# Performance work log

Measured on AMD Instinct MI355X. Metric: run time of the kernel, lower is better.

Reference implementation:

```python
import jax, jax.numpy as jnp
import numpy as np


def _lin_relu(V, W, b):
    # LinearEmbedding: matmul + bias + ReLU (with_act_func=True default)
    return jax.nn.relu(jnp.matmul(V, W) + b)


def setup_inputs() -> dict:
    key = jax.random.key(0)
    ks = jax.random.split(key, 8)
    B, N, F = 4, 4096, 512
    C = F // 8
    sx = 1.0 / np.sqrt(F)
    return {
        "V": jax.random.normal(ks[0], (B, N, F), dtype=jnp.float32),
        "Wf": jax.random.normal(ks[1], (F, C), dtype=jnp.float32) * sx,
        "bf": jax.random.normal(ks[2], (C,), dtype=jnp.float32) * 5e-5 + 1e-4,
        "Wg": jax.random.normal(ks[3], (F, C), dtype=jnp.float32) * sx,
        "bg": jax.random.normal(ks[4], (C,), dtype=jnp.float32) * 5e-5 + 1e-4,
        "Wh": jax.random.normal(ks[5], (F, F), dtype=jnp.float32) * sx,
        "bh": jax.random.normal(ks[6], (F,), dtype=jnp.float32) * 5e-5 + 1e-4,
        "gamma": jax.random.normal(ks[7], (F,), dtype=jnp.float32),
    }


def reference(V, Wf, bf, Wg, bg, Wh, bh, gamma):
    f_out = _lin_relu(V, Wf, bf)          # [B, N, C]
    g_out = _lin_relu(V, Wg, bg)          # [B, N, C]
    h_out = _lin_relu(V, Wh, bh)          # [B, N, F]
    scores = jnp.einsum('bnc,bmc->bnm', f_out, g_out)  # [B, N, N]
    s = jax.nn.softmax(scores, axis=-1)
    o = jnp.einsum('bnm,bmf->bnf', s, h_out)            # [B, N, F]
    return gamma * o + V
```

## Files before the change

kernel.cpp:

```cpp
#include <hip/hip_runtime.h>
#include <hip/hip_bf16.h>
#include <math.h>

#define M_ROWS 16384
#define F_DIM 512
#define C_DIM 64

typedef short bf16x8 __attribute__((ext_vector_type(8)));
typedef float floatx4 __attribute__((ext_vector_type(4)));
typedef unsigned short ushortx8 __attribute__((ext_vector_type(8)));
typedef unsigned short ushortx4 __attribute__((ext_vector_type(4)));

static __device__ __forceinline__ unsigned short f2bf(float x) {
    __hip_bfloat16 h = __float2bfloat16(x);
    return *reinterpret_cast<unsigned short*>(&h);
}
static __device__ __forceinline__ float bf2f(unsigned short h) {
    unsigned int u = ((unsigned int)h) << 16;
    return __builtin_bit_cast(float, u);
}

static __device__ __forceinline__ void lgkm_barrier() {
    asm volatile("s_waitcnt lgkmcnt(0)\n\ts_barrier" ::: "memory");
}


__global__ __launch_bounds__(64) void prep_w_kernel(
    const float* __restrict__ Wf, const float* __restrict__ Wg,
    const float* __restrict__ Wh,
    unsigned short* __restrict__ wt_hi, unsigned short* __restrict__ wt_lo)
{
    const int c = blockIdx.x;
    const int t = threadIdx.x;
    const float* W; int ld, cl;
    if (c < 64)       { W = Wf; ld = C_DIM; cl = c; }
    else if (c < 128) { W = Wg; ld = C_DIM; cl = c - 64; }
    else              { W = Wh; ld = F_DIM; cl = c - 128; }
    const int ng = c >> 4, l16 = c & 15;
    for (int k = t; k < F_DIM; k += 64) {
        const float x = W[(size_t)k * ld + cl];
        const unsigned short h = f2bf(x);
        const int kh = k >> 5, qd = (k >> 3) & 3, j = k & 7;
        const size_t off = (((size_t)(ng * 16 + kh) * 64) + qd * 16 + l16) * 8 + j;
        wt_hi[off] = h;
        wt_lo[off] = f2bf(x - bf2f(h));
    }
}

#define BM 64
#define LDK 72

__global__ __launch_bounds__(256, 4) void embed_mfma_kernel(
    const float* __restrict__ V,
    const unsigned short* __restrict__ wt_hi, const unsigned short* __restrict__ wt_lo,
    const float* __restrict__ bf, const float* __restrict__ bg,
    const float* __restrict__ bh,
    unsigned short* __restrict__ f_bf, unsigned short* __restrict__ g_bf,
    unsigned short* __restrict__ h_sw)
{
    __shared__ __align__(16) unsigned short a_hi[BM][LDK];
    __shared__ __align__(16) unsigned short a_lo[BM][LDK];

    const int t  = threadIdx.x;
    const int R0 = blockIdx.x * BM;
    const bool fg = (blockIdx.y == 0);
    const int cbase = fg ? 0 : blockIdx.y * 128;

    const int w = t >> 6, lane = t & 63, quad = lane >> 4, l16 = lane & 15;

    floatx4 acc[4][2];
    #pragma unroll
    for (int rt = 0; rt < 4; ++rt)
        #pragma unroll
        for (int c = 0; c < 2; ++c)
            acc[rt][c] = (floatx4){0.f, 0.f, 0.f, 0.f};

    const int arow = t >> 4;
    const int acol = (t & 15) * 4;
    const int ng0  = (cbase >> 4) + w * 2;

    #pragma unroll 1
    for (int k0 = 0; k0 < F_DIM; k0 += 64) {
        lgkm_barrier();
        #pragma unroll
        for (int rr = 0; rr < 4; ++rr) {
            const int row = rr * 16 + arow;
            const float4 x = *(const float4*)(V + (size_t)(R0 + row) * F_DIM + k0 + acol);
            const float xs[4] = {x.x, x.y, x.z, x.w};
            ushortx4 hi, lo;
            #pragma unroll
            for (int jj = 0; jj < 4; ++jj) {
                const unsigned short hb2 = f2bf(xs[jj]);
                hi[jj] = hb2;
                lo[jj] = f2bf(xs[jj] - bf2f(hb2));
            }
            *(ushortx4*)&a_hi[row][acol] = hi;
            if (fg) *(ushortx4*)&a_lo[row][acol] = lo;
        }
        lgkm_barrier();
        #pragma unroll
        for (int kk = 0; kk < 2; ++kk) {
            const int kh = (k0 >> 5) + kk;
            const bf16x8 b0 = *(const bf16x8*)(wt_hi + (((size_t)(ng0 * 16 + kh)) * 64 + lane) * 8);
            const bf16x8 b1 = *(const bf16x8*)(wt_hi + (((size_t)((ng0 + 1) * 16 + kh)) * 64 + lane) * 8);
            bf16x8 ah[4];
            #pragma unroll
            for (int rt = 0; rt < 4; ++rt)
                ah[rt] = *(const bf16x8*)&a_hi[rt * 16 + l16][kk * 32 + quad * 8];
            #pragma unroll
            for (int rt = 0; rt < 4; ++rt) {
                acc[rt][0] = __builtin_amdgcn_mfma_f32_16x16x32_bf16(ah[rt], b0, acc[rt][0], 0, 0, 0);
                acc[rt][1] = __builtin_amdgcn_mfma_f32_16x16x32_bf16(ah[rt], b1, acc[rt][1], 0, 0, 0);
            }
            if (fg) {
                const bf16x8 c0 = *(const bf16x8*)(wt_lo + (((size_t)(ng0 * 16 + kh)) * 64 + lane) * 8);
                const bf16x8 c1 = *(const bf16x8*)(wt_lo + (((size_t)((ng0 + 1) * 16 + kh)) * 64 + lane) * 8);
                bf16x8 al[4];
                #pragma unroll
                for (int rt = 0; rt < 4; ++rt)
                    al[rt] = *(const bf16x8*)&a_lo[rt * 16 + l16][kk * 32 + quad * 8];
                #pragma unroll
                for (int rt = 0; rt < 4; ++rt) {
                    acc[rt][0] = __builtin_amdgcn_mfma_f32_16x16x32_bf16(ah[rt], c0, acc[rt][0], 0, 0, 0);
                    acc[rt][0] = __builtin_amdgcn_mfma_f32_16x16x32_bf16(al[rt], b0, acc[rt][0], 0, 0, 0);
                    acc[rt][1] = __builtin_amdgcn_mfma_f32_16x16x32_bf16(ah[rt], c1, acc[rt][1], 0, 0, 0);
                    acc[rt][1] = __builtin_amdgcn_mfma_f32_16x16x32_bf16(al[rt], b1, acc[rt][1], 0, 0, 0);
                }
            }
        }
    }

    #pragma unroll
    for (int rt = 0; rt < 4; ++rt) {
        #pragma unroll
        for (int c = 0; c < 2; ++c) {
            const int wtc  = cbase + w * 32 + c * 16 + l16;
            const int rowl = rt * 16 + quad * 4;
            const float bias = fg ? (wtc < 64 ? bf[wtc] : bg[wtc - 64]) : bh[wtc - 128];
            const floatx4 v = acc[rt][c];
            if (fg) {
                unsigned short* dst = (wtc < 64) ? (f_bf + wtc) : (g_bf + wtc - 64);
                #pragma unroll
                for (int r = 0; r < 4; ++r) {
                    const float z = v[r] + bias;
                    dst[(size_t)(R0 + rowl + r) * C_DIM] = f2bf(z > 0.f ? z : 0.f);
                }
            } else {
                const int hc   = wtc - 128;
                const int grow = R0 + rowl;
                const int b    = grow >> 12, rl = grow & 4095;
                const int T    = rl >> 6, mloc = rl & 63;
                const int kh2  = mloc >> 5, q2 = (mloc >> 3) & 3, j0 = mloc & 7;
                ushortx4 st;
                #pragma unroll
                for (int r = 0; r < 4; ++r) {
                    const float z = v[r] + bias;
                    st[r] = f2bf(z > 0.f ? z : 0.f);
                }
                const size_t off = ((((size_t)(b * 64 + T) * 64) + (hc >> 4) * 2 + kh2) * 64
                                    + q2 * 16 + (hc & 15)) * 8 + j0;
                *(ushortx4*)(h_sw + off) = st;
            }
        }
    }
}

#define QT 128
#define KT 64
#define PST 72
#define GST 72

__global__ __launch_bounds__(1024, 4) void attn_mfma_kernel(
    const unsigned short* __restrict__ f_bf, const unsigned short* __restrict__ g_bf,
    const unsigned short* __restrict__ h_sw,
    unsigned short* __restrict__ O_ws, float* __restrict__ l_ws)
{
    __shared__ __align__(16) unsigned short p_lds[2][QT][PST];
    __shared__ __align__(16) unsigned short g_lds[2][KT][GST];
    __shared__ __align__(16) float l_half[2][QT];

    const int t = threadIdx.x;
    const int w = t >> 6, lane = t & 63, quad = lane >> 4, l16 = lane & 15;
    const int sr = (w & 7) * 16, sc = (w >> 3) * 32;

    const int bid = blockIdx.x;
    const int b   = (bid & 7) >> 1;
    const int j   = ((bid >> 3) << 1) | (bid & 1);
    const int qb  = j >> 1;
    const int ms  = j & 1;
    const int R0  = qb * QT;
    const int M0  = ms * 2048;

    const unsigned short* fb = f_bf + ((size_t)b * 4096 + R0) * C_DIM;
    const unsigned short* gb = g_bf + ((size_t)b * 4096 + M0) * C_DIM;
    const unsigned short* hbase = h_sw + (size_t)(b * 64 + ms * 32) * 32768;

    bf16x8 f0, f1;
    {
        const unsigned short* fr = fb + (size_t)(sr + l16) * C_DIM + quad * 8;
        f0 = *(const bf16x8*)fr;
        f1 = *(const bf16x8*)(fr + 32);
    }

    floatx4 acc[8][2];
    #pragma unroll
    for (int rt = 0; rt < 8; ++rt)
        #pragma unroll
        for (int c = 0; c < 2; ++c)
            acc[rt][c] = (floatx4){0.f, 0.f, 0.f, 0.f};
    float run_l[4] = {0.f, 0.f, 0.f, 0.f};

    const int grow = t >> 4, gk = (t & 15) * 4;
    ushortx4 greg = *(const ushortx4*)(gb + (size_t)grow * C_DIM + gk);

    for (int it = 0; it < 32; ++it) {
        const int buf = it & 1;
        const unsigned short* ht = hbase + (size_t)it * 32768 + (size_t)(4 * w) * 512;

        const bf16x8 h0 = *(const bf16x8*)(ht + (size_t)lane * 8);
        const bf16x8 h1 = *(const bf16x8*)(ht + 512 + (size_t)lane * 8);
        const bf16x8 h2 = *(const bf16x8*)(ht + 1024 + (size_t)lane * 8);
        const bf16x8 h3 = *(const bf16x8*)(ht + 1536 + (size_t)lane * 8);

        *(ushortx4*)&g_lds[buf][grow][gk] = greg;
        if (it < 31)
            greg = *(const ushortx4*)(gb + (size_t)((it + 1) * KT + grow) * C_DIM + gk);
        lgkm_barrier();

        #pragma unroll
        for (int ct = 0; ct < 2; ++ct) {
            const unsigned short* gr = &g_lds[buf][sc + ct * 16 + l16][quad * 8];
            const bf16x8 g0 = *(const bf16x8*)gr;
            const bf16x8 g1 = *(const bf16x8*)(gr + 32);
            floatx4 cc = (floatx4){0.f, 0.f, 0.f, 0.f};
            cc = __builtin_amdgcn_mfma_f32_16x16x32_bf16(f0, g0, cc, 0, 0, 0);
            cc = __builtin_amdgcn_mfma_f32_16x16x32_bf16(f1, g1, cc, 0, 0, 0);
            #pragma unroll
            for (int r = 0; r < 4; ++r) {
                const float p = __expf(cc[r] - 32.f);
                run_l[r] += p;
                p_lds[buf][sr + quad * 4 + r][sc + ct * 16 + l16] = f2bf(p);
            }
        }
        lgkm_barrier();

        #pragma unroll
        for (int rt = 0; rt < 8; ++rt) {
            const unsigned short* pr = &p_lds[buf][rt * 16 + l16][quad * 8];
            const bf16x8 pf0 = *(const bf16x8*)pr;
            const bf16x8 pf1 = *(const bf16x8*)(pr + 32);
            acc[rt][0] = __builtin_amdgcn_mfma_f32_16x16x32_bf16(pf0, h0, acc[rt][0], 0, 0, 0);
            acc[rt][0] = __builtin_amdgcn_mfma_f32_16x16x32_bf16(pf1, h1, acc[rt][0], 0, 0, 0);
            acc[rt][1] = __builtin_amdgcn_mfma_f32_16x16x32_bf16(pf0, h2, acc[rt][1], 0, 0, 0);
            acc[rt][1] = __builtin_amdgcn_mfma_f32_16x16x32_bf16(pf1, h3, acc[rt][1], 0, 0, 0);
        }
    }

    #pragma unroll
    for (int r = 0; r < 4; ++r) {
        float v = run_l[r];
        #pragma unroll
        for (int off = 1; off < 16; off <<= 1)
            v += __shfl_xor(v, off, 64);
        if (l16 == 0) l_half[w >> 3][sr + quad * 4 + r] = v;
    }
    __syncthreads();
    if (t < QT)
        l_ws[((size_t)(b * 2 + ms)) * 4096 + R0 + t] = l_half[0][t] + l_half[1][t];

    unsigned short* ob = O_ws + ((size_t)(b * 2 + ms) * 4096 + R0) * F_DIM;
    #pragma unroll
    for (int rt = 0; rt < 8; ++rt) {
        #pragma unroll
        for (int c = 0; c < 2; ++c) {
            const int col = w * 32 + c * 16 + l16;
            #pragma unroll
            for (int r = 0; r < 4; ++r) {
                const int row = rt * 16 + quad * 4 + r;
                ob[(size_t)row * F_DIM + col] = f2bf(acc[rt][c][r]);
            }
        }
    }
}

__global__ __launch_bounds__(256) void reduce_kernel(
    const unsigned short* __restrict__ O_ws, const float* __restrict__ l_ws,
    const float* __restrict__ gamma, const float* __restrict__ V,
    float* __restrict__ out)
{
    const size_t idx = ((size_t)blockIdx.x * 256 + threadIdx.x) * 8;
    const int row = (int)(idx >> 9);
    const int col = (int)(idx & 511);
    const int b = row >> 12, rb = row & 4095;

    const ushortx8 o0 = *(const ushortx8*)(O_ws + ((size_t)(b * 2 + 0) * 4096 + rb) * F_DIM + col);
    const ushortx8 o1 = *(const ushortx8*)(O_ws + ((size_t)(b * 2 + 1) * 4096 + rb) * F_DIM + col);
    const float linv = 1.f / (l_ws[(size_t)(b * 2 + 0) * 4096 + rb] +
                              l_ws[(size_t)(b * 2 + 1) * 4096 + rb]);
    const float4 ga = *(const float4*)(gamma + col);
    const float4 gb2 = *(const float4*)(gamma + col + 4);
    const float4 v0 = *(const float4*)(V + idx);
    const float4 v1 = *(const float4*)(V + idx + 4);

    float4 r0, r1;
    r0.x = ga.x  * ((bf2f(o0[0]) + bf2f(o1[0])) * linv) + v0.x;
    r0.y = ga.y  * ((bf2f(o0[1]) + bf2f(o1[1])) * linv) + v0.y;
    r0.z = ga.z  * ((bf2f(o0[2]) + bf2f(o1[2])) * linv) + v0.z;
    r0.w = ga.w  * ((bf2f(o0[3]) + bf2f(o1[3])) * linv) + v0.w;
    r1.x = gb2.x * ((bf2f(o0[4]) + bf2f(o1[4])) * linv) + v1.x;
    r1.y = gb2.y * ((bf2f(o0[5]) + bf2f(o1[5])) * linv) + v1.y;
    r1.z = gb2.z * ((bf2f(o0[6]) + bf2f(o1[6])) * linv) + v1.z;
    r1.w = gb2.w * ((bf2f(o0[7]) + bf2f(o1[7])) * linv) + v1.w;
    *(float4*)(out + idx)     = r0;
    *(float4*)(out + idx + 4) = r1;
}

extern "C" void kernel_launch(void* const* d_in, const int* in_sizes, int n_in,
                              void* d_out, int out_size, void* d_ws, size_t ws_size,
                              hipStream_t stream) {
    const float* V     = (const float*)d_in[0];
    const float* Wf    = (const float*)d_in[1];
    const float* bf    = (const float*)d_in[2];
    const float* Wg    = (const float*)d_in[3];
    const float* bg    = (const float*)d_in[4];
    const float* Wh    = (const float*)d_in[5];
    const float* bh    = (const float*)d_in[6];
    const float* gamma = (const float*)d_in[7];
    float* out = (float*)d_out;

    unsigned short* f_bf  = (unsigned short*)d_ws;
    unsigned short* g_bf  = f_bf + (size_t)M_ROWS * C_DIM;
    unsigned short* h_sw  = g_bf + (size_t)M_ROWS * C_DIM;
    unsigned short* wt_hi = h_sw + (size_t)4 * F_DIM * 4096;
    unsigned short* wt_lo = wt_hi + (size_t)640 * F_DIM;
    unsigned short* O_ws  = wt_lo + (size_t)640 * F_DIM;
    float*          l_ws  = (float*)(O_ws + (size_t)8 * 4096 * F_DIM);

    prep_w_kernel<<<640, 64, 0, stream>>>(Wf, Wg, Wh, wt_hi, wt_lo);
    embed_mfma_kernel<<<dim3(M_ROWS / BM, 5), 256, 0, stream>>>(
        V, wt_hi, wt_lo, bf, bg, bh, f_bf, g_bf, h_sw);
    attn_mfma_kernel<<<256, 1024, 0, stream>>>(f_bf, g_bf, h_sw, O_ws, l_ws);
    reduce_kernel<<<M_ROWS * F_DIM / (256 * 8), 256, 0, stream>>>(
        O_ws, l_ws, gamma, V, out);
}
```

Measured before the change: 205.7 us.

## Drop key split, fuse normalization and residual into attention, swizzle LDS

The attention kernel no longer splits the key dimension into two halves. Each block now takes 64 query rows and walks all 4096 keys, so the partial O/l workspace and the separate reduce kernel go away, and gamma scaling plus the V residual are done in the attention epilogue. The padded LDS layouts are replaced with XOR-swizzled layouts to avoid bank conflicts. Each block now reads h twice as many times relative to the output it produces, and the output stores are scattered 4-byte writes, in exchange for removing the bf16 O round trip through memory and one launch.

```diff
diff --git a/kernel.cpp b/kernel.cpp
--- a/kernel.cpp
+++ b/kernel.cpp
@@ -165,55 +165,58 @@
     }
 }
 
-#define QT 128
+#define QT 64
 #define KT 64
-#define PST 72
-#define GST 72
 
 __global__ __launch_bounds__(1024, 4) void attn_mfma_kernel(
     const unsigned short* __restrict__ f_bf, const unsigned short* __restrict__ g_bf,
-    const unsigned short* __restrict__ h_sw,
-    unsigned short* __restrict__ O_ws, float* __restrict__ l_ws)
+    const unsigned short* __restrict__ h_sw, const float* __restrict__ gamma,
+    const float* __restrict__ V, float* __restrict__ out)
 {
-    __shared__ __align__(16) unsigned short p_lds[2][QT][PST];
-    __shared__ __align__(16) unsigned short g_lds[2][KT][GST];
-    __shared__ __align__(16) float l_half[2][QT];
+    __shared__ __align__(16) unsigned short p_lds[2][QT * 64];
+    __shared__ __align__(16) unsigned short g_lds[2][KT * 64];
+    __shared__ float l_red[4][QT];
+    __shared__ float l_inv[QT];
 
     const int t = threadIdx.x;
     const int w = t >> 6, lane = t & 63, quad = lane >> 4, l16 = lane & 15;
-    const int sr = (w & 7) * 16, sc = (w >> 3) * 32;
-
-    const int bid = blockIdx.x;
-    const int b   = (bid & 7) >> 1;
-    const int j   = ((bid >> 3) << 1) | (bid & 1);
-    const int qb  = j >> 1;
-    const int ms  = j & 1;
-    const int R0  = qb * QT;
-    const int M0  = ms * 2048;
-
-    const unsigned short* fb = f_bf + ((size_t)b * 4096 + R0) * C_DIM;
-    const unsigned short* gb = g_bf + ((size_t)b * 4096 + M0) * C_DIM;
-    const unsigned short* hbase = h_sw + (size_t)(b * 64 + ms * 32) * 32768;
+    const int wr = w & 3, wc = w >> 2;
+
+    const int bid  = blockIdx.x;
+    const int orig = (bid & 7) * 32 + (bid >> 3);
+    const int b    = orig >> 6, qb = orig & 63;
+    const int R0   = qb * QT;
+
+    const unsigned short* fb    = f_bf + ((size_t)b * 4096 + R0) * C_DIM;
+    const unsigned short* gb    = g_bf + (size_t)b * 4096 * C_DIM;
+    const unsigned short* hbase = h_sw + (size_t)b * 64 * 32768;
 
     bf16x8 f0, f1;
     {
-        const unsigned short* fr = fb + (size_t)(sr + l16) * C_DIM + quad * 8;
+        const unsigned short* fr = fb + (size_t)(wr * 16 + l16) * C_DIM + quad * 8;
         f0 = *(const bf16x8*)fr;
         f1 = *(const bf16x8*)(fr + 32);
     }
-
-    floatx4 acc[8][2];
-    #pragma unroll
-    for (int rt = 0; rt < 8; ++rt)
+    const float gam0 = gamma[w * 32 + l16];
+    const float gam1 = gamma[w * 32 + 16 + l16];
+
+    floatx4 acc[4][2];
+    #pragma unroll
+    for (int rt = 0; rt < 4; ++rt)
         #pragma unroll
         for (int c = 0; c < 2; ++c)
             acc[rt][c] = (floatx4){0.f, 0.f, 0.f, 0.f};
     float run_l[4] = {0.f, 0.f, 0.f, 0.f};
 
-    const int grow = t >> 4, gk = (t & 15) * 4;
+    const int grow    = t >> 4, gk = (t & 15) * 4;
+    const int g_swoff = grow * 128 + ((gk * 2) ^ ((grow & 7) << 4));
     ushortx4 greg = *(const ushortx4*)(gb + (size_t)grow * C_DIM + gk);
 
-    for (int it = 0; it < 32; ++it) {
+    const int sgrow   = wc * 16 + l16;
+    const int sg_off0 = sgrow * 128 + ((quad * 16)      ^ ((sgrow & 7) << 4));
+    const int sg_off1 = sgrow * 128 + ((quad * 16 + 64) ^ ((sgrow & 7) << 4));
+
+    for (int it = 0; it < 64; ++it) {
         const int buf = it & 1;
         const unsigned short* ht = hbase + (size_t)it * 32768 + (size_t)(4 * w) * 512;
 
@@ -222,16 +225,17 @@
         const bf16x8 h2 = *(const bf16x8*)(ht + 1024 + (size_t)lane * 8);
         const bf16x8 h3 = *(const bf16x8*)(ht + 1536 + (size_t)lane * 8);
 
-        *(ushortx4*)&g_lds[buf][grow][gk] = greg;
-        if (it < 31)
+        *(ushortx4*)((unsigned char*)&g_lds[buf][0] + g_swoff) = greg;
+        if (it < 63)
             greg = *(const ushortx4*)(gb + (size_t)((it + 1) * KT + grow) * C_DIM + gk);
         lgkm_barrier();
 
-        #pragma unroll
-        for (int ct = 0; ct < 2; ++ct) {
-            const unsigned short* gr = &g_lds[buf][sc + ct * 16 + l16][quad * 8];
-            const bf16x8 g0 = *(const bf16x8*)gr;
-            const bf16x8 g1 = *(const bf16x8*)(gr + 32);
+        const unsigned char* gB = (const unsigned char*)&g_lds[buf][0];
+        unsigned char*       pB = (unsigned char*)&p_lds[buf][0];
+
+        {
+            const bf16x8 g0 = *(const bf16x8*)(gB + sg_off0);
+            const bf16x8 g1 = *(const bf16x8*)(gB + sg_off1);
             floatx4 cc = (floatx4){0.f, 0.f, 0.f, 0.f};
             cc = __builtin_amdgcn_mfma_f32_16x16x32_bf16(f0, g0, cc, 0, 0, 0);
             cc = __builtin_amdgcn_mfma_f32_16x16x32_bf16(f1, g1, cc, 0, 0, 0);
@@ -239,16 +243,19 @@
             for (int r = 0; r < 4; ++r) {
                 const float p = __expf(cc[r] - 32.f);
                 run_l[r] += p;
-                p_lds[buf][sr + quad * 4 + r][sc + ct * 16 + l16] = f2bf(p);
+                const int prow = wr * 16 + quad * 4 + r;
+                const int pcol = wc * 16 + l16;
+                *(unsigned short*)(pB + prow * 128 + ((pcol * 2) ^ ((prow & 7) << 4))) = f2bf(p);
             }
         }
         lgkm_barrier();
 
         #pragma unroll
-        for (int rt = 0; rt < 8; ++rt) {
-            const unsigned short* pr = &p_lds[buf][rt * 16 + l16][quad * 8];
-            const bf16x8 pf0 = *(const bf16x8*)pr;
-            const bf16x8 pf1 = *(const bf16x8*)(pr + 32);
+        for (int rt = 0; rt < 4; ++rt) {
+            const int prow = rt * 16 + l16;
+            const int sw   = (prow & 7) << 4;
+            const bf16x8 pf0 = *(const bf16x8*)(pB + prow * 128 + ((quad * 16)      ^ sw));
+            const bf16x8 pf1 = *(const bf16x8*)(pB + prow * 128 + ((quad * 16 + 64) ^ sw));
             acc[rt][0] = __builtin_amdgcn_mfma_f32_16x16x32_bf16(pf0, h0, acc[rt][0], 0, 0, 0);
             acc[rt][0] = __builtin_amdgcn_mfma_f32_16x16x32_bf16(pf1, h1, acc[rt][0], 0, 0, 0);
             acc[rt][1] = __builtin_amdgcn_mfma_f32_16x16x32_bf16(pf0, h2, acc[rt][1], 0, 0, 0);
@@ -259,60 +266,30 @@
     #pragma unroll
     for (int r = 0; r < 4; ++r) {
         float v = run_l[r];
-        #pragma unroll
-        for (int off = 1; off < 16; off <<= 1)
-            v += __shfl_xor(v, off, 64);
-        if (l16 == 0) l_half[w >> 3][sr + quad * 4 + r] = v;
+        v += __shfl_xor(v, 1, 64);
+        v += __shfl_xor(v, 2, 64);
+        v += __shfl_xor(v, 4, 64);
+        v += __shfl_xor(v, 8, 64);
+        if (l16 == 0) l_red[wc][wr * 16 + quad * 4 + r] = v;
     }
     __syncthreads();
     if (t < QT)
-        l_ws[((size_t)(b * 2 + ms)) * 4096 + R0 + t] = l_half[0][t] + l_half[1][t];
-
-    unsigned short* ob = O_ws + ((size_t)(b * 2 + ms) * 4096 + R0) * F_DIM;
-    #pragma unroll
-    for (int rt = 0; rt < 8; ++rt) {
-        #pragma unroll
-        for (int c = 0; c < 2; ++c) {
-            const int col = w * 32 + c * 16 + l16;
-            #pragma unroll
-            for (int r = 0; r < 4; ++r) {
-                const int row = rt * 16 + quad * 4 + r;
-                ob[(size_t)row * F_DIM + col] = f2bf(acc[rt][c][r]);
-            }
-        }
-    }
-}
-
-__global__ __launch_bounds__(256) void reduce_kernel(
-    const unsigned short* __restrict__ O_ws, const float* __restrict__ l_ws,
-    const float* __restrict__ gamma, const float* __restrict__ V,
-    float* __restrict__ out)
-{
-    const size_t idx = ((size_t)blockIdx.x * 256 + threadIdx.x) * 8;
-    const int row = (int)(idx >> 9);
-    const int col = (int)(idx & 511);
-    const int b = row >> 12, rb = row & 4095;
-
-    const ushortx8 o0 = *(const ushortx8*)(O_ws + ((size_t)(b * 2 + 0) * 4096 + rb) * F_DIM + col);
-    const ushortx8 o1 = *(const ushortx8*)(O_ws + ((size_t)(b * 2 + 1) * 4096 + rb) * F_DIM + col);
-    const float linv = 1.f / (l_ws[(size_t)(b * 2 + 0) * 4096 + rb] +
-                              l_ws[(size_t)(b * 2 + 1) * 4096 + rb]);
-    const float4 ga = *(const float4*)(gamma + col);
-    const float4 gb2 = *(const float4*)(gamma + col + 4);
-    const float4 v0 = *(const float4*)(V + idx);
-    const float4 v1 = *(const float4*)(V + idx + 4);
-
-    float4 r0, r1;
-    r0.x = ga.x  * ((bf2f(o0[0]) + bf2f(o1[0])) * linv) + v0.x;
-    r0.y = ga.y  * ((bf2f(o0[1]) + bf2f(o1[1])) * linv) + v0.y;
-    r0.z = ga.z  * ((bf2f(o0[2]) + bf2f(o1[2])) * linv) + v0.z;
-    r0.w = ga.w  * ((bf2f(o0[3]) + bf2f(o1[3])) * linv) + v0.w;
-    r1.x = gb2.x * ((bf2f(o0[4]) + bf2f(o1[4])) * linv) + v1.x;
-    r1.y = gb2.y * ((bf2f(o0[5]) + bf2f(o1[5])) * linv) + v1.y;
-    r1.z = gb2.z * ((bf2f(o0[6]) + bf2f(o1[6])) * linv) + v1.z;
-    r1.w = gb2.w * ((bf2f(o0[7]) + bf2f(o1[7])) * linv) + v1.w;
-    *(float4*)(out + idx)     = r0;
-    *(float4*)(out + idx + 4) = r1;
+        l_inv[t] = 1.f / (l_red[0][t] + l_red[1][t] + l_red[2][t] + l_red[3][t]);
+    __syncthreads();
+
+    const float* Vb = V   + ((size_t)b * 4096 + R0) * F_DIM;
+    float*       ob = out + ((size_t)b * 4096 + R0) * F_DIM;
+    const int c0 = w * 32 + l16;
+    #pragma unroll
+    for (int rt = 0; rt < 4; ++rt) {
+        #pragma unroll
+        for (int r = 0; r < 4; ++r) {
+            const int row = rt * 16 + quad * 4 + r;
+            const float li = l_inv[row];
+            ob[(size_t)row * F_DIM + c0]      = gam0 * acc[rt][0][r] * li + Vb[(size_t)row * F_DIM + c0];
+            ob[(size_t)row * F_DIM + c0 + 16] = gam1 * acc[rt][1][r] * li + Vb[(size_t)row * F_DIM + c0 + 16];
+        }
+    }
 }
 
 extern "C" void kernel_launch(void* const* d_in, const int* in_sizes, int n_in,
@@ -333,13 +310,9 @@
     unsigned short* h_sw  = g_bf + (size_t)M_ROWS * C_DIM;
     unsigned short* wt_hi = h_sw + (size_t)4 * F_DIM * 4096;
     unsigned short* wt_lo = wt_hi + (size_t)640 * F_DIM;
-    unsigned short* O_ws  = wt_lo + (size_t)640 * F_DIM;
-    float*          l_ws  = (float*)(O_ws + (size_t)8 * 4096 * F_DIM);
 
     prep_w_kernel<<<640, 64, 0, stream>>>(Wf, Wg, Wh, wt_hi, wt_lo);
     embed_mfma_kernel<<<dim3(M_ROWS / BM, 5), 256, 0, stream>>>(
         V, wt_hi, wt_lo, bf, bg, bh, f_bf, g_bf, h_sw);
-    attn_mfma_kernel<<<256, 1024, 0, stream>>>(f_bf, g_bf, h_sw, O_ws, l_ws);
-    reduce_kernel<<<M_ROWS * F_DIM / (256 * 8), 256, 0, stream>>>(
-        O_ws, l_ws, gamma, V, out);
-}
+    attn_mfma_kernel<<<256, 1024, 0, stream>>>(f_bf, g_bf, h_sw, gamma, V, out);
+}
```

Result: no change. 203.5 us (-1.1%).
